# Performance work log

Hardware: AMD Instinct MI355X
Metric: run time of the kernel (lower is better)

Reference implementation:

```python
import jax, jax.numpy as jnp
import numpy as np

N_NODES = 50000
N_EDGES = 600000
F_IN = 128   # nfeature
H = 128      # nhidden (must equal nfeature due to original code's gcn2 init)
C = 10       # nclass


def setup_inputs() -> dict:
    key = jax.random.key(0)
    ks = jax.random.split(key, 8)
    row = jax.random.randint(ks[0], (N_EDGES,), 0, N_NODES)
    col = jax.random.randint(ks[1], (N_EDGES,), 0, N_NODES)
    label = jax.random.randint(ks[2], (N_EDGES,), 0, C)
    features = jax.random.normal(ks[3], (N_NODES, F_IN), dtype=jnp.float32)
    s1 = 1.0 / np.sqrt(F_IN)
    W1 = jax.random.uniform(ks[4], (H, F_IN), jnp.float32, -s1, s1)
    b1 = jnp.zeros((H,), jnp.float32)
    s2 = 1.0 / np.sqrt(H)
    W2 = jax.random.uniform(ks[5], (H, H), jnp.float32, -s2, s2)
    b2 = jnp.zeros((H,), jnp.float32)
    s3 = 1.0 / np.sqrt(2 * H)
    Wfc = jax.random.uniform(ks[6], (C, 2 * H), jnp.float32, -s3, s3)
    bfc = jnp.zeros((C,), jnp.float32)
    return {"features": features, "W1": W1, "b1": b1, "W2": W2, "b2": b2,
            "Wfc": Wfc, "bfc": bfc, "row": row, "col": col, "label": label}


def gcn_conv(x, row, col, W, b):
    # GCNConv: add self loops, linear, then deg-normalized scatter-add.
    n = x.shape[0]
    sl = jnp.arange(n, dtype=row.dtype)
    r = jnp.concatenate([row, sl])  # source / j index (PyG edge_index[0])
    c = jnp.concatenate([col, sl])  # target / aggregation index (edge_index[1])
    h = x @ W.T + b  # [N, H]
    # degree computed over row of self-loop-augmented edge_index (>=1 always)
    deg = jax.ops.segment_sum(jnp.ones(r.shape, h.dtype), r, num_segments=n)
    dinv = deg ** -0.5
    norm = dinv[r] * dinv[c]  # [E+N]
    msg = norm[:, None] * h[r]  # gather + scale, [E+N, H]
    return jax.ops.segment_sum(msg, c, num_segments=n)  # scatter-add, [N, H]


def reference(features, W1, b1, W2, b2, Wfc, bfc, row, col, label):
    h1 = gcn_conv(features, row, col, W1, b1)  # [N, H]
    h2 = gcn_conv(h1, row, col, W2, b2)        # [N, H]
    # take_logits: index_select per edge endpoint, concat on feature dim
    x = jnp.concatenate([h2[row], h2[col]], axis=1)  # [E, 2H]
    logits = x @ Wfc.T + bfc  # [E, C]
    logp = jax.nn.log_softmax(logits, axis=-1)
    loss = -jnp.mean(jnp.take_along_axis(logp, label[:, None], axis=1))
    return loss, logits
```

## Files before the change

kernel.cpp:

```cpp
#include <hip/hip_runtime.h>
#include <hip/hip_bf16.h>
#include <math.h>

#define NND 50000
#define NE  600000
#define HD  128
#define NC  10
#define CAP 64
#define SCATB 256
#define GEMMB 782
#define LOSSB 2344

typedef unsigned short ushort_t;
typedef unsigned char uchar_t;
typedef __attribute__((ext_vector_type(8))) short short8;
typedef __attribute__((ext_vector_type(4))) float f32x4;

__device__ __forceinline__ float bf2f(unsigned short u) {
  return __uint_as_float(((unsigned int)u) << 16);
}
__device__ __forceinline__ unsigned short f2bf(float f) {
  __hip_bfloat16 h = __float2bfloat16(f);
  return *(unsigned short*)&h;
}

__device__ __forceinline__ short8 f2bf8(const float* __restrict__ p) {
  float4 x0 = *(const float4*)p;
  float4 x1 = *(const float4*)(p + 4);
  short8 v;
  v[0] = (short)f2bf(x0.x); v[1] = (short)f2bf(x0.y);
  v[2] = (short)f2bf(x0.z); v[3] = (short)f2bf(x0.w);
  v[4] = (short)f2bf(x1.x); v[5] = (short)f2bf(x1.y);
  v[6] = (short)f2bf(x1.z); v[7] = (short)f2bf(x1.w);
  return v;
}

template <bool FP32IN>
__device__ __forceinline__ void gemm_body_w(const void* __restrict__ Xv,
                                            const float* __restrict__ W,
                                            const float* __restrict__ b,
                                            ushort_t* __restrict__ Y,
                                            ushort_t* Bs, int bid, int tid) {
  for (int idx = tid; idx < 2048; idx += 256) {
    int g = idx >> 6, lane = idx & 63;
    int nt = g >> 2, t = g & 3;
    int n = nt * 16 + (lane & 15), q = (lane >> 4) & 3;
    *(short8*)&Bs[idx * 8] = f2bf8(&W[n * HD + t * 32 + q * 8]);
  }
  __syncthreads();
  int w = tid >> 6, lane = tid & 63;
  int m = lane & 15, q = lane >> 4;
  int rowbase = bid * 64 + w * 16;
  int rm = rowbase + m; if (rm >= NND) rm = NND - 1;
  short8 a[4];
  if (FP32IN) {
    const float* X = (const float*)Xv;
    #pragma unroll
    for (int t = 0; t < 4; t++)
      a[t] = f2bf8(&X[(long)rm * HD + t * 32 + q * 8]);
  } else {
    const ushort_t* X = (const ushort_t*)Xv;
    #pragma unroll
    for (int t = 0; t < 4; t++)
      a[t] = *(const short8*)&X[(long)rm * HD + t * 32 + q * 8];
  }
  #pragma unroll
  for (int nt = 0; nt < 8; nt++) {
    f32x4 acc = {0.f, 0.f, 0.f, 0.f};
    #pragma unroll
    for (int t = 0; t < 4; t++) {
      short8 bf = *(const short8*)&Bs[((nt * 4 + t) * 64 + lane) * 8];
      acc = __builtin_amdgcn_mfma_f32_16x16x32_bf16(a[t], bf, acc, 0, 0, 0);
    }
    float bias = b[nt * 16 + m];
    #pragma unroll
    for (int reg = 0; reg < 4; reg++) {
      int r = rowbase + q * 4 + reg;
      if (r < NND) Y[(long)r * HD + nt * 16 + m] = f2bf(acc[reg] + bias);
    }
  }
}

__global__ __launch_bounds__(256) void k_front(const int* __restrict__ row,
                                               const int* __restrict__ col,
                                               int* __restrict__ pos,
                                               int* __restrict__ deg,
                                               int* __restrict__ srcs,
                                               const float* __restrict__ features,
                                               const float* __restrict__ W1,
                                               const float* __restrict__ b1,
                                               ushort_t* __restrict__ Y,
                                               float* __restrict__ out) {
  __shared__ ushort_t Bs[16384];
  int tid = threadIdx.x, bb = blockIdx.x;
  if (bb < SCATB) {
    if (bb == 0 && tid == 0) out[0] = 0.f;
    int stride = SCATB * 256;
    for (int e = bb * 256 + tid; e < NE; e += stride) {
      int c = col[e], r = row[e];
      int slot = atomicAdd(&pos[c], 1);
      if (slot < CAP) srcs[(size_t)c * CAP + slot] = r;
      atomicAdd(&deg[r], 1);
    }
  } else {
    gemm_body_w<true>((const void*)features, W1, b1, Y, Bs, bb - SCATB, tid);
  }
}

__global__ __launch_bounds__(256) void k_aggr(const ushort_t* __restrict__ H,
                                              const int* __restrict__ srcs,
                                              const int* __restrict__ pos,
                                              const int* __restrict__ deg,
                                              ushort_t* __restrict__ O) {
  int g = threadIdx.x >> 5, lane = threadIdx.x & 31;
  int half = lane >> 4;
  int fl = (lane & 15) * 8;
  int node = blockIdx.x * 8 + g;
  if (node >= NND) return;
  float di = rsqrtf(1.0f + (float)deg[node]);
  short8 hv = *(const short8*)&H[(long)node * HD + fl];
  float acc[8];
  float sw = (half == 0) ? di * di : 0.0f;
  #pragma unroll
  for (int j = 0; j < 8; j++) acc[j] = sw * bf2f((unsigned short)hv[j]);
  int cnt = pos[node]; if (cnt > CAP) cnt = CAP;
  const int* nb = &srcs[(long)node * CAP];
  for (int base = 0; base < cnt; base += 32) {
    int m = cnt - base; if (m > 32) m = 32;
    int sl = 0; float wl = 0.f;
    if (lane < m) { sl = nb[base + lane]; wl = di * rsqrtf(1.0f + (float)deg[sl]); }
    int iters = (m + 1) >> 1;
    int u = 0;
    for (; u + 1 < iters; u += 2) {
      int t0 = 2 * u + half, t1 = t0 + 2;
      int s0 = __shfl(sl, t0 & 31, 32); float w0 = __shfl(wl, t0 & 31, 32);
      int s1 = __shfl(sl, t1 & 31, 32); float w1 = __shfl(wl, t1 & 31, 32);
      short8 h0 = *(const short8*)&H[(long)s0 * HD + fl];
      short8 h1 = *(const short8*)&H[(long)s1 * HD + fl];
      #pragma unroll
      for (int j = 0; j < 8; j++) acc[j] += w0 * bf2f((unsigned short)h0[j]);
      #pragma unroll
      for (int j = 0; j < 8; j++) acc[j] += w1 * bf2f((unsigned short)h1[j]);
    }
    if (u < iters) {
      int t = 2 * u + half;
      int s = __shfl(sl, t & 31, 32); float w = __shfl(wl, t & 31, 32);
      short8 hs = *(const short8*)&H[(long)s * HD + fl];
      #pragma unroll
      for (int j = 0; j < 8; j++) acc[j] += w * bf2f((unsigned short)hs[j]);
    }
  }
  #pragma unroll
  for (int j = 0; j < 8; j++) acc[j] += __shfl(acc[j], (lane & 15) + 16, 32);
  if (half == 0) {
    short8 r;
    #pragma unroll
    for (int j = 0; j < 8; j++) r[j] = (short)f2bf(acc[j]);
    *(short8*)&O[(long)node * HD + fl] = r;
  }
}

__global__ __launch_bounds__(256) void k_gemm2q(const ushort_t* __restrict__ X,
                                                const float* __restrict__ W2,
                                                const float* __restrict__ b,
                                                const float* __restrict__ Wfc,
                                                ushort_t* __restrict__ Q) {
  __shared__ ushort_t Bs[16384];
  __shared__ ushort_t Ts[4 * 16 * 136];
  int tid = threadIdx.x;
  for (int idx = tid; idx < 2048; idx += 256) {
    int g = idx >> 6, lane2 = idx & 63;
    int nt = g >> 2, t = g & 3;
    int n2 = nt * 16 + (lane2 & 15), q2 = (lane2 >> 4) & 3;
    *(short8*)&Bs[idx * 8] = f2bf8(&W2[n2 * HD + t * 32 + q2 * 8]);
  }
  __syncthreads();
  int w = tid >> 6, lane = tid & 63;
  int m = lane & 15, q = lane >> 4;
  int rowbase = blockIdx.x * 64 + w * 16;
  int rm = rowbase + m; if (rm >= NND) rm = NND - 1;
  short8 a[4];
  #pragma unroll
  for (int t = 0; t < 4; t++)
    a[t] = *(const short8*)&X[(long)rm * HD + t * 32 + q * 8];
  ushort_t* Tw = &Ts[w * 2176];
  #pragma unroll
  for (int nt = 0; nt < 8; nt++) {
    f32x4 acc = {0.f, 0.f, 0.f, 0.f};
    #pragma unroll
    for (int t = 0; t < 4; t++) {
      short8 bf = *(const short8*)&Bs[((nt * 4 + t) * 64 + lane) * 8];
      acc = __builtin_amdgcn_mfma_f32_16x16x32_bf16(a[t], bf, acc, 0, 0, 0);
    }
    float bias = b[nt * 16 + m];
    #pragma unroll
    for (int reg = 0; reg < 4; reg++)
      Tw[(q * 4 + reg) * 136 + nt * 16 + m] = f2bf(acc[reg] + bias);
  }
  short8 a2[4];
  #pragma unroll
  for (int t = 0; t < 4; t++)
    a2[t] = *(const short8*)&Tw[m * 136 + t * 32 + q * 8];
  f32x4 aL = {0.f, 0.f, 0.f, 0.f}, aR = {0.f, 0.f, 0.f, 0.f};
  #pragma unroll
  for (int t = 0; t < 8; t++) {
    short8 bv = {0, 0, 0, 0, 0, 0, 0, 0};
    if (m < NC) bv = f2bf8(&Wfc[m * 256 + t * 32 + q * 8]);
    if (t < 4) aL = __builtin_amdgcn_mfma_f32_16x16x32_bf16(a2[t], bv, aL, 0, 0, 0);
    else       aR = __builtin_amdgcn_mfma_f32_16x16x32_bf16(a2[t & 3], bv, aR, 0, 0, 0);
  }
  if (m < 12) {
    #pragma unroll
    for (int reg = 0; reg < 4; reg++) {
      int r = rowbase + q * 4 + reg;
      if (r < NND) {
        Q[(long)r * 24 + m]      = f2bf(aL[reg]);
        Q[(long)r * 24 + 12 + m] = f2bf(aR[reg]);
      }
    }
  }
}

__global__ __launch_bounds__(256) void k_aggr2(const ushort_t* __restrict__ Q,
                                               const int* __restrict__ srcs,
                                               const int* __restrict__ pos,
                                               const int* __restrict__ deg,
                                               float* __restrict__ Pr,
                                               float* __restrict__ Pc) {
  int g = threadIdx.x >> 5, lane = threadIdx.x & 31;
  int half = lane >> 4;
  int f = lane & 15;
  int node = blockIdx.x * 8 + g;
  if (node >= NND) return;
  float di = rsqrtf(1.0f + (float)deg[node]);
  bool act = (f < 12);
  unsigned int qv = act ? *(const unsigned int*)&Q[(long)node * 24 + 2 * f] : 0u;
  float sw = (half == 0) ? di * di : 0.f;
  float a0 = sw * bf2f((ushort_t)(qv & 0xffff));
  float a1 = sw * bf2f((ushort_t)(qv >> 16));
  int cnt = pos[node]; if (cnt > CAP) cnt = CAP;
  const int* nb = &srcs[(long)node * CAP];
  for (int base = 0; base < cnt; base += 32) {
    int m2 = cnt - base; if (m2 > 32) m2 = 32;
    int sl = 0; float wl = 0.f;
    if (lane < m2) { sl = nb[base + lane]; wl = di * rsqrtf(1.0f + (float)deg[sl]); }
    int iters = (m2 + 1) >> 1;
    int u = 0;
    for (; u + 1 < iters; u += 2) {
      int t0 = 2 * u + half, t1 = t0 + 2;
      int s0 = __shfl(sl, t0 & 31, 32); float w0 = __shfl(wl, t0 & 31, 32);
      int s1 = __shfl(sl, t1 & 31, 32); float w1 = __shfl(wl, t1 & 31, 32);
      unsigned int h0 = act ? *(const unsigned int*)&Q[(long)s0 * 24 + 2 * f] : 0u;
      unsigned int h1 = act ? *(const unsigned int*)&Q[(long)s1 * 24 + 2 * f] : 0u;
      a0 += w0 * bf2f((ushort_t)(h0 & 0xffff));
      a1 += w0 * bf2f((ushort_t)(h0 >> 16));
      a0 += w1 * bf2f((ushort_t)(h1 & 0xffff));
      a1 += w1 * bf2f((ushort_t)(h1 >> 16));
    }
    if (u < iters) {
      int t = 2 * u + half;
      int s = __shfl(sl, t & 31, 32); float wv = __shfl(wl, t & 31, 32);
      unsigned int hs = act ? *(const unsigned int*)&Q[(long)s * 24 + 2 * f] : 0u;
      a0 += wv * bf2f((ushort_t)(hs & 0xffff));
      a1 += wv * bf2f((ushort_t)(hs >> 16));
    }
  }
  a0 += __shfl(a0, f + 16, 32);
  a1 += __shfl(a1, f + 16, 32);
  if (half == 0 && act) {
    float2 v; v.x = a0; v.y = a1;
    if (f < 6) *(float2*)&Pr[(long)node * 12 + 2 * f] = v;
    else       *(float2*)&Pc[(long)node * 12 + 2 * (f - 6)] = v;
  }
}

__global__ __launch_bounds__(256) void k_edge(const float* __restrict__ Pr,
                                              const float* __restrict__ Pc,
                                              const int* __restrict__ row,
                                              const int* __restrict__ col,
                                              const int* __restrict__ label,
                                              const float* __restrict__ bfc,
                                              float* __restrict__ logits,
                                              float* __restrict__ out) {
  __shared__ __align__(16) float S[2560];
  __shared__ float Ls[4];
  int tid = threadIdx.x;
  long e0 = (long)blockIdx.x * 256;
  int e = (int)e0 + tid;
  float lp = 0.f;
  if (e < NE) {
    int r = row[e], c = col[e];
    const float* pr = &Pr[(long)r * 12];
    const float* pc = &Pc[(long)c * 12];
    float4 r0 = *(const float4*)&pr[0];
    float4 r1 = *(const float4*)&pr[4];
    float4 r2 = *(const float4*)&pr[8];
    float4 c0 = *(const float4*)&pc[0];
    float4 c1 = *(const float4*)&pc[4];
    float4 c2 = *(const float4*)&pc[8];
    float p[NC];
    p[0] = r0.x + c0.x + bfc[0]; p[1] = r0.y + c0.y + bfc[1];
    p[2] = r0.z + c0.z + bfc[2]; p[3] = r0.w + c0.w + bfc[3];
    p[4] = r1.x + c1.x + bfc[4]; p[5] = r1.y + c1.y + bfc[5];
    p[6] = r1.z + c1.z + bfc[6]; p[7] = r1.w + c1.w + bfc[7];
    p[8] = r2.x + c2.x + bfc[8]; p[9] = r2.y + c2.y + bfc[9];
    #pragma unroll
    for (int cc = 0; cc < NC; cc++) S[tid * 10 + cc] = p[cc];
    float mx = p[0];
    #pragma unroll
    for (int cc = 1; cc < NC; cc++) mx = fmaxf(mx, p[cc]);
    float se = 0.f;
    #pragma unroll
    for (int cc = 0; cc < NC; cc++) se += __expf(p[cc] - mx);
    int lb = label[e];
    float plb = p[0];
    #pragma unroll
    for (int cc = 1; cc < NC; cc++) plb = (cc == lb) ? p[cc] : plb;
    lp = plb - mx - __logf(se);
  }
  __syncthreads();
  int ve = NE - (int)e0; if (ve > 256) ve = 256;
  int limF4 = ve * 10 / 4;
  float4* dst = (float4*)&logits[e0 * 10];
  const float4* src4 = (const float4*)S;
  for (int i = tid; i < limF4; i += 256) dst[i] = src4[i];
  #pragma unroll
  for (int off = 32; off > 0; off >>= 1) lp += __shfl_xor(lp, off, 64);
  if ((tid & 63) == 0) Ls[tid >> 6] = lp;
  __syncthreads();
  if (tid == 0)
    atomicAdd(out, -(Ls[0] + Ls[1] + Ls[2] + Ls[3]) / (float)NE);
}

extern "C" void kernel_launch(void* const* d_in, const int* in_sizes, int n_in,
                              void* d_out, int out_size, void* d_ws, size_t ws_size,
                              hipStream_t stream) {
  const float* features = (const float*)d_in[0];
  const float* W1  = (const float*)d_in[1];
  const float* b1  = (const float*)d_in[2];
  const float* W2  = (const float*)d_in[3];
  const float* b2  = (const float*)d_in[4];
  const float* Wfc = (const float*)d_in[5];
  const float* bfc = (const float*)d_in[6];
  const int* row   = (const int*)d_in[7];
  const int* col   = (const int*)d_in[8];
  const int* label = (const int*)d_in[9];
  float* out = (float*)d_out;

  int* pos = (int*)d_ws;
  int* deg = pos + 50048;
  int* srcs = deg + 50048;
  float* Pr = (float*)(srcs + (size_t)NND * CAP);
  float* Pc = Pr + 600000;
  ushort_t* bufA = (ushort_t*)(Pc + 600000);
  ushort_t* bufB = bufA + 6400000;
  ushort_t* Q = bufA;

  hipMemsetAsync(pos, 0, 2 * 50048 * sizeof(int), stream);
  k_front<<<SCATB + GEMMB, 256, 0, stream>>>(row, col, pos, deg, srcs,
                                             features, W1, b1, bufA, out);
  k_aggr<<<6250, 256, 0, stream>>>(bufA, srcs, pos, deg, bufB);
  k_gemm2q<<<GEMMB, 256, 0, stream>>>(bufB, W2, b2, Wfc, Q);
  k_aggr2<<<6250, 256, 0, stream>>>(Q, srcs, pos, deg, Pr, Pc);
  k_edge<<<LOSSB, 256, 0, stream>>>(Pr, Pc, row, col, label, bfc, out + 1, out);
}
```

Before: 240.5 us.

## Fold W1, W2 and Wfc into one projection before both aggregations

Uses linearity of GCN aggregation to precompute M = Wfc·W2·W1 (20x128) in a prep kernel, so features are projected to 20 columns up front. Both aggregation passes then move 24-wide bf16 rows instead of 128-wide ones, and bias terms are corrected with a ones-column and a self-value term. The change also stores neighbour indices as 16-bit values, replaces the memset with zeroing blocks inside the prep kernel, and doubles the number of scatter blocks. Risks: projected values are rounded to bf16 at a different point, and the 16-bit indices only hold while node ids stay below 65536.

```diff
diff --git a/kernel.cpp b/kernel.cpp
--- a/kernel.cpp
+++ b/kernel.cpp
@@ -7,12 +7,12 @@
 #define HD  128
 #define NC  10
 #define CAP 64
-#define SCATB 256
+#define SCATB 512
 #define GEMMB 782
 #define LOSSB 2344
+#define ZEROB 98
 
 typedef unsigned short ushort_t;
-typedef unsigned char uchar_t;
 typedef __attribute__((ext_vector_type(8))) short short8;
 typedef __attribute__((ext_vector_type(4))) float f32x4;
 
@@ -35,49 +35,62 @@
   return v;
 }
 
-template <bool FP32IN>
-__device__ __forceinline__ void gemm_body_w(const void* __restrict__ Xv,
-                                            const float* __restrict__ W,
-                                            const float* __restrict__ b,
-                                            ushort_t* __restrict__ Y,
-                                            ushort_t* Bs, int bid, int tid) {
-  for (int idx = tid; idx < 2048; idx += 256) {
+__global__ __launch_bounds__(256) void k_prep(const float* __restrict__ W1,
+                                              const float* __restrict__ W2,
+                                              const float* __restrict__ Wfc,
+                                              const float* __restrict__ b1,
+                                              const float* __restrict__ b2,
+                                              ushort_t* __restrict__ Bf,
+                                              float* __restrict__ uv,
+                                              int* __restrict__ posdeg,
+                                              float* __restrict__ out) {
+  int tid = threadIdx.x;
+  if (blockIdx.x > 0) {
+    for (int k = (blockIdx.x - 1) * 256 + tid; k < 2 * 50048; k += ZEROB * 256)
+      posdeg[k] = 0;
+    return;
+  }
+  if (tid == 0) out[0] = 0.f;
+  __shared__ float V[20][128];
+  __shared__ float M[20][128];
+  for (int o = tid; o < 20 * 128; o += 256) {
+    int c = o >> 7, k = o & 127;
+    int cc = (c < 10) ? c : c - 10;
+    const float* wrow = &Wfc[cc * 256 + ((c < 10) ? 0 : 128)];
+    float s = 0.f;
+    for (int m2 = 0; m2 < 128; m2++) s += wrow[m2] * W2[m2 * HD + k];
+    V[c][k] = s;
+  }
+  __syncthreads();
+  for (int o = tid; o < 20 * 128; o += 256) {
+    int c = o >> 7, j = o & 127;
+    float s = 0.f;
+    for (int k = 0; k < 128; k++) s += V[c][k] * W1[k * HD + j];
+    M[c][j] = s;
+  }
+  __syncthreads();
+  for (int idx = tid; idx < 512; idx += 256) {
     int g = idx >> 6, lane = idx & 63;
     int nt = g >> 2, t = g & 3;
-    int n = nt * 16 + (lane & 15), q = (lane >> 4) & 3;
-    *(short8*)&Bs[idx * 8] = f2bf8(&W[n * HD + t * 32 + q * 8]);
-  }
-  __syncthreads();
-  int w = tid >> 6, lane = tid & 63;
-  int m = lane & 15, q = lane >> 4;
-  int rowbase = bid * 64 + w * 16;
-  int rm = rowbase + m; if (rm >= NND) rm = NND - 1;
-  short8 a[4];
-  if (FP32IN) {
-    const float* X = (const float*)Xv;
-    #pragma unroll
-    for (int t = 0; t < 4; t++)
-      a[t] = f2bf8(&X[(long)rm * HD + t * 32 + q * 8]);
-  } else {
-    const ushort_t* X = (const ushort_t*)Xv;
-    #pragma unroll
-    for (int t = 0; t < 4; t++)
-      a[t] = *(const short8*)&X[(long)rm * HD + t * 32 + q * 8];
-  }
-  #pragma unroll
-  for (int nt = 0; nt < 8; nt++) {
-    f32x4 acc = {0.f, 0.f, 0.f, 0.f};
-    #pragma unroll
-    for (int t = 0; t < 4; t++) {
-      short8 bf = *(const short8*)&Bs[((nt * 4 + t) * 64 + lane) * 8];
-      acc = __builtin_amdgcn_mfma_f32_16x16x32_bf16(a[t], bf, acc, 0, 0, 0);
-    }
-    float bias = b[nt * 16 + m];
-    #pragma unroll
-    for (int reg = 0; reg < 4; reg++) {
-      int r = rowbase + q * 4 + reg;
-      if (r < NND) Y[(long)r * HD + nt * 16 + m] = f2bf(acc[reg] + bias);
-    }
+    int n = lane & 15, q = (lane >> 4) & 3;
+    int kb = t * 32 + q * 8;
+    #pragma unroll
+    for (int j = 0; j < 8; j++) {
+      float s = (n < 10) ? M[nt * 10 + n][kb + j] : 0.f;
+      Bf[idx * 8 + j] = f2bf(s);
+    }
+  }
+  if (tid < 20) {
+    float s = 0.f;
+    for (int k = 0; k < 128; k++) s += V[tid][k] * b1[k];
+    uv[tid] = s;
+  } else if (tid < 40) {
+    int c = tid - 20;
+    int cc = (c < 10) ? c : c - 10;
+    const float* wrow = &Wfc[cc * 256 + ((c < 10) ? 0 : 128)];
+    float s = 0.f;
+    for (int k = 0; k < 128; k++) s += wrow[k] * b2[k];
+    uv[tid] = s;
   }
 }
 
@@ -85,148 +98,62 @@
                                                const int* __restrict__ col,
                                                int* __restrict__ pos,
                                                int* __restrict__ deg,
-                                               int* __restrict__ srcs,
+                                               ushort_t* __restrict__ srcs,
                                                const float* __restrict__ features,
-                                               const float* __restrict__ W1,
-                                               const float* __restrict__ b1,
-                                               ushort_t* __restrict__ Y,
-                                               float* __restrict__ out) {
-  __shared__ ushort_t Bs[16384];
+                                               const ushort_t* __restrict__ Bf,
+                                               ushort_t* __restrict__ T0) {
   int tid = threadIdx.x, bb = blockIdx.x;
   if (bb < SCATB) {
-    if (bb == 0 && tid == 0) out[0] = 0.f;
     int stride = SCATB * 256;
     for (int e = bb * 256 + tid; e < NE; e += stride) {
       int c = col[e], r = row[e];
       int slot = atomicAdd(&pos[c], 1);
-      if (slot < CAP) srcs[(size_t)c * CAP + slot] = r;
+      if (slot < CAP) srcs[(size_t)c * CAP + slot] = (ushort_t)r;
       atomicAdd(&deg[r], 1);
     }
   } else {
-    gemm_body_w<true>((const void*)features, W1, b1, Y, Bs, bb - SCATB, tid);
-  }
-}
-
-__global__ __launch_bounds__(256) void k_aggr(const ushort_t* __restrict__ H,
-                                              const int* __restrict__ srcs,
-                                              const int* __restrict__ pos,
-                                              const int* __restrict__ deg,
-                                              ushort_t* __restrict__ O) {
-  int g = threadIdx.x >> 5, lane = threadIdx.x & 31;
-  int half = lane >> 4;
-  int fl = (lane & 15) * 8;
-  int node = blockIdx.x * 8 + g;
-  if (node >= NND) return;
-  float di = rsqrtf(1.0f + (float)deg[node]);
-  short8 hv = *(const short8*)&H[(long)node * HD + fl];
-  float acc[8];
-  float sw = (half == 0) ? di * di : 0.0f;
-  #pragma unroll
-  for (int j = 0; j < 8; j++) acc[j] = sw * bf2f((unsigned short)hv[j]);
-  int cnt = pos[node]; if (cnt > CAP) cnt = CAP;
-  const int* nb = &srcs[(long)node * CAP];
-  for (int base = 0; base < cnt; base += 32) {
-    int m = cnt - base; if (m > 32) m = 32;
-    int sl = 0; float wl = 0.f;
-    if (lane < m) { sl = nb[base + lane]; wl = di * rsqrtf(1.0f + (float)deg[sl]); }
-    int iters = (m + 1) >> 1;
-    int u = 0;
-    for (; u + 1 < iters; u += 2) {
-      int t0 = 2 * u + half, t1 = t0 + 2;
-      int s0 = __shfl(sl, t0 & 31, 32); float w0 = __shfl(wl, t0 & 31, 32);
-      int s1 = __shfl(sl, t1 & 31, 32); float w1 = __shfl(wl, t1 & 31, 32);
-      short8 h0 = *(const short8*)&H[(long)s0 * HD + fl];
-      short8 h1 = *(const short8*)&H[(long)s1 * HD + fl];
+    int bid = bb - SCATB;
+    int w = tid >> 6, lane = tid & 63;
+    int m = lane & 15, q = lane >> 4;
+    short8 B[8];
+    #pragma unroll
+    for (int g = 0; g < 8; g++) B[g] = *(const short8*)&Bf[(g * 64 + lane) * 8];
+    int rowbase = bid * 64 + w * 16;
+    int rm = rowbase + m; if (rm >= NND) rm = NND - 1;
+    short8 a[4];
+    #pragma unroll
+    for (int t = 0; t < 4; t++)
+      a[t] = f2bf8(&features[(long)rm * HD + t * 32 + q * 8]);
+    f32x4 accL = {0.f, 0.f, 0.f, 0.f}, accR = {0.f, 0.f, 0.f, 0.f};
+    #pragma unroll
+    for (int t = 0; t < 4; t++) {
+      accL = __builtin_amdgcn_mfma_f32_16x16x32_bf16(a[t], B[t],     accL, 0, 0, 0);
+      accR = __builtin_amdgcn_mfma_f32_16x16x32_bf16(a[t], B[4 + t], accR, 0, 0, 0);
+    }
+    if (m < 12) {
       #pragma unroll
-      for (int j = 0; j < 8; j++) acc[j] += w0 * bf2f((unsigned short)h0[j]);
-      #pragma unroll
-      for (int j = 0; j < 8; j++) acc[j] += w1 * bf2f((unsigned short)h1[j]);
-    }
-    if (u < iters) {
-      int t = 2 * u + half;
-      int s = __shfl(sl, t & 31, 32); float w = __shfl(wl, t & 31, 32);
-      short8 hs = *(const short8*)&H[(long)s * HD + fl];
-      #pragma unroll
-      for (int j = 0; j < 8; j++) acc[j] += w * bf2f((unsigned short)hs[j]);
-    }
-  }
-  #pragma unroll
-  for (int j = 0; j < 8; j++) acc[j] += __shfl(acc[j], (lane & 15) + 16, 32);
-  if (half == 0) {
-    short8 r;
-    #pragma unroll
-    for (int j = 0; j < 8; j++) r[j] = (short)f2bf(acc[j]);
-    *(short8*)&O[(long)node * HD + fl] = r;
-  }
-}
-
-__global__ __launch_bounds__(256) void k_gemm2q(const ushort_t* __restrict__ X,
-                                                const float* __restrict__ W2,
-                                                const float* __restrict__ b,
-                                                const float* __restrict__ Wfc,
-                                                ushort_t* __restrict__ Q) {
-  __shared__ ushort_t Bs[16384];
-  __shared__ ushort_t Ts[4 * 16 * 136];
-  int tid = threadIdx.x;
-  for (int idx = tid; idx < 2048; idx += 256) {
-    int g = idx >> 6, lane2 = idx & 63;
-    int nt = g >> 2, t = g & 3;
-    int n2 = nt * 16 + (lane2 & 15), q2 = (lane2 >> 4) & 3;
-    *(short8*)&Bs[idx * 8] = f2bf8(&W2[n2 * HD + t * 32 + q2 * 8]);
-  }
-  __syncthreads();
-  int w = tid >> 6, lane = tid & 63;
-  int m = lane & 15, q = lane >> 4;
-  int rowbase = blockIdx.x * 64 + w * 16;
-  int rm = rowbase + m; if (rm >= NND) rm = NND - 1;
-  short8 a[4];
-  #pragma unroll
-  for (int t = 0; t < 4; t++)
-    a[t] = *(const short8*)&X[(long)rm * HD + t * 32 + q * 8];
-  ushort_t* Tw = &Ts[w * 2176];
-  #pragma unroll
-  for (int nt = 0; nt < 8; nt++) {
-    f32x4 acc = {0.f, 0.f, 0.f, 0.f};
-    #pragma unroll
-    for (int t = 0; t < 4; t++) {
-      short8 bf = *(const short8*)&Bs[((nt * 4 + t) * 64 + lane) * 8];
-      acc = __builtin_amdgcn_mfma_f32_16x16x32_bf16(a[t], bf, acc, 0, 0, 0);
-    }
-    float bias = b[nt * 16 + m];
-    #pragma unroll
-    for (int reg = 0; reg < 4; reg++)
-      Tw[(q * 4 + reg) * 136 + nt * 16 + m] = f2bf(acc[reg] + bias);
-  }
-  short8 a2[4];
-  #pragma unroll
-  for (int t = 0; t < 4; t++)
-    a2[t] = *(const short8*)&Tw[m * 136 + t * 32 + q * 8];
-  f32x4 aL = {0.f, 0.f, 0.f, 0.f}, aR = {0.f, 0.f, 0.f, 0.f};
-  #pragma unroll
-  for (int t = 0; t < 8; t++) {
-    short8 bv = {0, 0, 0, 0, 0, 0, 0, 0};
-    if (m < NC) bv = f2bf8(&Wfc[m * 256 + t * 32 + q * 8]);
-    if (t < 4) aL = __builtin_amdgcn_mfma_f32_16x16x32_bf16(a2[t], bv, aL, 0, 0, 0);
-    else       aR = __builtin_amdgcn_mfma_f32_16x16x32_bf16(a2[t & 3], bv, aR, 0, 0, 0);
-  }
-  if (m < 12) {
-    #pragma unroll
-    for (int reg = 0; reg < 4; reg++) {
-      int r = rowbase + q * 4 + reg;
-      if (r < NND) {
-        Q[(long)r * 24 + m]      = f2bf(aL[reg]);
-        Q[(long)r * 24 + 12 + m] = f2bf(aR[reg]);
+      for (int reg = 0; reg < 4; reg++) {
+        int r = rowbase + q * 4 + reg;
+        if (r < NND) {
+          float vL = (m < 10) ? accL[reg] : ((m == 10) ? 1.0f : 0.0f);
+          float vR = (m < 10) ? accR[reg] : 0.0f;
+          T0[(long)r * 24 + m]      = f2bf(vL);
+          T0[(long)r * 24 + 12 + m] = f2bf(vR);
+        }
       }
     }
   }
 }
 
-__global__ __launch_bounds__(256) void k_aggr2(const ushort_t* __restrict__ Q,
-                                               const int* __restrict__ srcs,
+template <bool FINAL>
+__global__ __launch_bounds__(256) void k_aggrn(const ushort_t* __restrict__ Q,
+                                               const ushort_t* __restrict__ srcs,
                                                const int* __restrict__ pos,
                                                const int* __restrict__ deg,
+                                               ushort_t* __restrict__ T1,
                                                float* __restrict__ Pr,
-                                               float* __restrict__ Pc) {
+                                               float* __restrict__ Pc,
+                                               const float* __restrict__ uv) {
   int g = threadIdx.x >> 5, lane = threadIdx.x & 31;
   int half = lane >> 4;
   int f = lane & 15;
@@ -239,11 +166,11 @@
   float a0 = sw * bf2f((ushort_t)(qv & 0xffff));
   float a1 = sw * bf2f((ushort_t)(qv >> 16));
   int cnt = pos[node]; if (cnt > CAP) cnt = CAP;
-  const int* nb = &srcs[(long)node * CAP];
+  const ushort_t* nb = &srcs[(long)node * CAP];
   for (int base = 0; base < cnt; base += 32) {
     int m2 = cnt - base; if (m2 > 32) m2 = 32;
     int sl = 0; float wl = 0.f;
-    if (lane < m2) { sl = nb[base + lane]; wl = di * rsqrtf(1.0f + (float)deg[sl]); }
+    if (lane < m2) { sl = (int)nb[base + lane]; wl = di * rsqrtf(1.0f + (float)deg[sl]); }
     int iters = (m2 + 1) >> 1;
     int u = 0;
     for (; u + 1 < iters; u += 2) {
@@ -267,10 +194,29 @@
   }
   a0 += __shfl(a0, f + 16, 32);
   a1 += __shfl(a1, f + 16, 32);
-  if (half == 0 && act) {
-    float2 v; v.x = a0; v.y = a1;
-    if (f < 6) *(float2*)&Pr[(long)node * 12 + 2 * f] = v;
-    else       *(float2*)&Pc[(long)node * 12 + 2 * (f - 6)] = v;
+  if (FINAL) {
+    float s_i = __shfl(bf2f((ushort_t)(qv & 0xffff)), 5, 32);
+    float z2  = __shfl(a0, 5, 32);
+    if (half == 0) {
+      if (f < 5) {
+        int cc = 2 * f;
+        float2 v;
+        v.x = a0 + z2 * uv[cc]     + s_i * uv[20 + cc];
+        v.y = a1 + z2 * uv[cc + 1] + s_i * uv[20 + cc + 1];
+        *(float2*)&Pr[(long)node * 12 + cc] = v;
+      } else if (f >= 6 && f < 11) {
+        int cc = 2 * f - 12;
+        float2 v;
+        v.x = a0 + z2 * uv[10 + cc]     + s_i * uv[30 + cc];
+        v.y = a1 + z2 * uv[10 + cc + 1] + s_i * uv[30 + cc + 1];
+        *(float2*)&Pc[(long)node * 12 + cc] = v;
+      }
+    }
+  } else {
+    if (half == 0 && act) {
+      unsigned int o = ((unsigned int)f2bf(a1) << 16) | (unsigned int)f2bf(a0);
+      *(unsigned int*)&T1[(long)node * 24 + 2 * f] = o;
+    }
   }
 }
 
@@ -347,20 +293,21 @@
   const int* label = (const int*)d_in[9];
   float* out = (float*)d_out;
 
-  int* pos = (int*)d_ws;
-  int* deg = pos + 50048;
-  int* srcs = deg + 50048;
-  float* Pr = (float*)(srcs + (size_t)NND * CAP);
-  float* Pc = Pr + 600000;
-  ushort_t* bufA = (ushort_t*)(Pc + 600000);
-  ushort_t* bufB = bufA + 6400000;
-  ushort_t* Q = bufA;
-
-  hipMemsetAsync(pos, 0, 2 * 50048 * sizeof(int), stream);
-  k_front<<<SCATB + GEMMB, 256, 0, stream>>>(row, col, pos, deg, srcs,
-                                             features, W1, b1, bufA, out);
-  k_aggr<<<6250, 256, 0, stream>>>(bufA, srcs, pos, deg, bufB);
-  k_gemm2q<<<GEMMB, 256, 0, stream>>>(bufB, W2, b2, Wfc, Q);
-  k_aggr2<<<6250, 256, 0, stream>>>(Q, srcs, pos, deg, Pr, Pc);
+  float* ws = (float*)d_ws;
+  size_t o = 0;
+  int* pos = (int*)(ws + o);        o += 50048;
+  int* deg = (int*)(ws + o);        o += 50048;
+  ushort_t* srcs = (ushort_t*)(ws + o); o += (size_t)NND * CAP / 2;
+  float* Pr = ws + o;               o += 600000;
+  float* Pc = ws + o;               o += 600000;
+  float* uv = ws + o;               o += 64;
+  ushort_t* Bf = (ushort_t*)(ws + o); o += 2048;
+  ushort_t* T0 = (ushort_t*)(ws + o); o += 600000;
+  ushort_t* T1 = (ushort_t*)(ws + o); o += 600000;
+
+  k_prep<<<1 + ZEROB, 256, 0, stream>>>(W1, W2, Wfc, b1, b2, Bf, uv, pos, out);
+  k_front<<<SCATB + GEMMB, 256, 0, stream>>>(row, col, pos, deg, srcs, features, Bf, T0);
+  k_aggrn<false><<<6250, 256, 0, stream>>>(T0, srcs, pos, deg, T1, nullptr, nullptr, uv);
+  k_aggrn<true><<<6250, 256, 0, stream>>>(T1, srcs, pos, deg, nullptr, Pr, Pc, uv);
   k_edge<<<LOSSB, 256, 0, stream>>>(Pr, Pc, row, col, label, bfc, out + 1, out);
 }
```

New measurement: 258.1 us. +7.3%, slower.
